# Performance work log

Measured on AMD Instinct MI355X. Metric: run time of the kernel, lower is better.

Reference implementation:

```python
import jax, jax.numpy as jnp
import numpy as np

B, T, C, H = 4, 4096, 1024, 16


def setup_inputs() -> dict:
    key = jax.random.key(0)
    k1, k2, k3 = jax.random.split(key, 3)
    x = jax.random.normal(k1, (B, T, C), dtype=jnp.float32)
    # nn.Linear(d_model, 3*d_model, bias=False): weight shape [3C, C]
    W_qkv = jax.random.normal(k2, (3 * C, C), dtype=jnp.float32) * 0.02
    # output Linear(d_model, d_model): weight [C, C], bias [C]
    W_out = jax.random.normal(k3, (C, C), dtype=jnp.float32) * 0.02
    b_out = jnp.zeros((C,), dtype=jnp.float32)
    return {"x": x, "W_qkv": W_qkv, "W_out": W_out, "b_out": b_out}


def reference(x, W_qkv, W_out, b_out):
    Bs, Ts, Cs = x.shape
    dh = Cs // H
    scale = dh ** (-0.5)
    # qkv projection: [B,T,3C]
    qkv = x @ W_qkv.T
    q, k, v = jnp.split(qkv, 3, axis=-1)

    def to_heads(t):  # [B,T,C] -> [B,H,T,dh]
        return t.reshape(Bs, Ts, H, dh).transpose(0, 2, 1, 3)

    q, k, v = to_heads(q), to_heads(k), to_heads(v)
    # rfft over the sequence dim -> [B,H,F,dh], F = T//2+1 (complex64)
    q_f = jnp.fft.rfft(q, axis=-2)
    k_f = jnp.fft.rfft(k, axis=-2)
    # spectral score: sum over head_dim of conj(q)*k, real part -> [B,H,F]
    attn = jnp.sum(jnp.conj(q_f) * k_f, axis=-1).real * scale
    attn = jax.nn.softmax(attn, axis=-1)  # softmax over frequency bins
    v_f = jnp.fft.rfft(v, axis=-2)
    out = jnp.fft.irfft(attn[..., None] * v_f, n=Ts, axis=-2)  # [B,H,T,dh]
    out = out.transpose(0, 2, 1, 3).reshape(Bs, Ts, Cs)
    # output projection (dropout is identity in eval)
    return out @ W_out.T + b_out
```

## Files before the change

kernel.cpp:

```cpp
#include <hip/hip_runtime.h>
#include <math.h>

#define Bsz   4
#define Tsz   4096
#define Csz   1024
#define Hn    16
#define DHn   64
#define NTOT  (Bsz * Tsz)
#define M3    (3 * Csz)
#define Fn    2049
#define BHn   (Bsz * Hn)
#define HALFN 8192

typedef __bf16 bf16x8 __attribute__((ext_vector_type(8)));
typedef __bf16 bf16x4 __attribute__((ext_vector_type(4)));
typedef float  f32x4  __attribute__((ext_vector_type(4)));

__device__ __forceinline__ void gload_lds16(const void* g, void* l) {
  __builtin_amdgcn_global_load_lds(
      (const __attribute__((address_space(1))) void*)g,
      (__attribute__((address_space(3))) void*)l, 16, 0, 0);
}

__global__ __launch_bounds__(256)
void cvt_hilo_kernel(const float4* __restrict__ in, bf16x4* __restrict__ hi,
                     bf16x4* __restrict__ lo, int n4) {
  int i = blockIdx.x * blockDim.x + threadIdx.x;
  if (i >= n4) return;
  float4 v = in[i];
  bf16x4 h, l;
  h[0] = (__bf16)v.x; h[1] = (__bf16)v.y; h[2] = (__bf16)v.z; h[3] = (__bf16)v.w;
  l[0] = (__bf16)(v.x - (float)h[0]);
  l[1] = (__bf16)(v.y - (float)h[1]);
  l[2] = (__bf16)(v.z - (float)h[2]);
  l[3] = (__bf16)(v.w - (float)h[3]);
  hi[i] = h;
  lo[i] = l;
}

__global__ __launch_bounds__(256)
void transpose_cvt_kernel(const float* __restrict__ src,
                          __bf16* __restrict__ hi, __bf16* __restrict__ lo) {
  __shared__ float tile[64][65];
  const int tid = threadIdx.x;
  const int n0 = blockIdx.x * 64;
  const int c0 = blockIdx.y * 64;
  const int col = tid & 63;
  const int row4 = tid >> 6;
#pragma unroll
  for (int i = 0; i < 16; ++i) {
    const int r = i * 4 + row4;
    tile[r][col] = src[(size_t)(c0 + r) * NTOT + n0 + col];
  }
  __syncthreads();
#pragma unroll
  for (int i = 0; i < 16; ++i) {
    const int n = i * 4 + row4;
    const float v = tile[col][n];
    const __bf16 h = (__bf16)v;
    const __bf16 l = (__bf16)(v - (float)h);
    hi[(size_t)(n0 + n) * Csz + c0 + col] = h;
    lo[(size_t)(n0 + n) * Csz + c0 + col] = l;
  }
}

template<int COLMAP>
__global__ __launch_bounds__(512, 2)
void gemm_8s(const __bf16* __restrict__ Ahi, const __bf16* __restrict__ Alo,
             const __bf16* __restrict__ Bhi, const __bf16* __restrict__ Blo,
             float* __restrict__ C, int ldC, int nbase,
             const float* __restrict__ bias) {
  __shared__ __align__(16) char lds[131072];

  const int tid  = threadIdx.x;
  const int wid  = tid >> 6;
  const int lane = tid & 63;
  const int wm = wid >> 2, wn = wid & 3;

  int bx = blockIdx.x, by = blockIdx.y;
  {
    const int gx = gridDim.x, gy = gridDim.y;
    const int nwg = gx * gy;
    if ((nwg & 7) == 0) {
      const int flat  = by * gx + bx;
      const int chunk = nwg >> 3;
      const int nf    = (flat & 7) * chunk + (flat >> 3);
      if (COLMAP) { bx = nf / gy; by = nf % gy; }
      else        { bx = nf % gx; by = nf / gx; }
    }
  }
  const int m0 = by * 256;
  const int n0 = bx * 256;

  const int r16 = lane & 15;
  const int kc  = lane >> 4;

  const int aq = (wid & 3) + ((wid & 4) ? 4 : 0);
  const int bq = ((wid & 3) << 1) + (wid >> 2);
  const __bf16* gAh = Ahi + (size_t)(m0 + (wid & 3) * 16 + ((wid & 4) ? 128 : 0) + r16) * Csz + kc * 8;
  const __bf16* gAl = Alo + (size_t)(m0 + (wid & 3) * 16 + ((wid & 4) ? 128 : 0) + r16) * Csz + kc * 8;
  const __bf16* gBh = Bhi + (size_t)(n0 + (wid & 3) * 64 + (wid >> 2) * 16 + r16) * Csz + kc * 8;
  const __bf16* gBl = Blo + (size_t)(n0 + (wid & 3) * 64 + (wid >> 2) * 16 + r16) * Csz + kc * 8;

  auto stA = [&](int h, int ts, char* slot) {
    const size_t o = (size_t)h * 64 * Csz + ts * 32;
    gload_lds16(gAh + o, slot + aq * 1024);
    gload_lds16(gAl + o, slot + 8192 + aq * 1024);
  };
  auto stB = [&](int h, int ts, char* slot) {
    const size_t o = (size_t)h * 32 * Csz + ts * 32;
    gload_lds16(gBh + o, slot + bq * 1024);
    gload_lds16(gBl + o, slot + 8192 + bq * 1024);
  };

  f32x4 acc[8][4];
#pragma unroll
  for (int i = 0; i < 8; ++i)
#pragma unroll
    for (int j = 0; j < 4; ++j) acc[i][j] = (f32x4)(0.f);

  stA(0, 0, lds);            stB(0, 0, lds + 16384);
  stB(1, 0, lds + 32768);    stA(1, 0, lds + 49152);
  stA(0, 1, lds + 65536);    stB(0, 1, lds + 81920);

#pragma unroll 1
  for (int t = 0; t < 32; ++t) {
    char* cur = lds + ((t & 1) << 16);
    char* nxt = lds + (((t & 1) ^ 1) << 16);
    bf16x8 ah[4], al[4], bh[4], bl[4];

    if (t < 31) asm volatile("s_waitcnt vmcnt(8)" ::: "memory");
    else        asm volatile("s_waitcnt vmcnt(4)" ::: "memory");
    __builtin_amdgcn_s_barrier();
#pragma unroll
    for (int f = 0; f < 4; ++f) {
      const int off = (wm * 4 + f) * 1024 + lane * 16;
      ah[f] = *(const bf16x8*)(cur + off);
      al[f] = *(const bf16x8*)(cur + 8192 + off);
    }
#pragma unroll
    for (int j = 0; j < 2; ++j) {
      const int off = ((wn << 1) + j) * 1024 + lane * 16;
      bh[j] = *(const bf16x8*)(cur + 16384 + off);
      bl[j] = *(const bf16x8*)(cur + 16384 + 8192 + off);
    }
    if (t < 31) stB(1, t + 1, nxt + 32768);
    asm volatile("s_waitcnt lgkmcnt(0)" ::: "memory");
    __builtin_amdgcn_sched_barrier(0);
    __builtin_amdgcn_s_setprio(1);
#pragma unroll
    for (int f = 0; f < 4; ++f)
#pragma unroll
      for (int j = 0; j < 2; ++j) {
        f32x4 a_ = acc[f][j];
        a_ = __builtin_amdgcn_mfma_f32_16x16x32_bf16(ah[f], bh[j], a_, 0, 0, 0);
        a_ = __builtin_amdgcn_mfma_f32_16x16x32_bf16(ah[f], bl[j], a_, 0, 0, 0);
        a_ = __builtin_amdgcn_mfma_f32_16x16x32_bf16(al[f], bh[j], a_, 0, 0, 0);
        acc[f][j] = a_;
      }
    __builtin_amdgcn_s_setprio(0);

    if (t < 31) asm volatile("s_waitcnt vmcnt(8)" ::: "memory");
    else        asm volatile("s_waitcnt vmcnt(2)" ::: "memory");
    __builtin_amdgcn_s_barrier();
#pragma unroll
    for (int j = 0; j < 2; ++j) {
      const int off = ((wn << 1) + j) * 1024 + lane * 16;
      bh[2 + j] = *(const bf16x8*)(cur + 32768 + off);
      bl[2 + j] = *(const bf16x8*)(cur + 32768 + 8192 + off);
    }
    if (t < 31) stA(1, t + 1, nxt + 49152);
    asm volatile("s_waitcnt lgkmcnt(0)" ::: "memory");
    __builtin_amdgcn_sched_barrier(0);
    __builtin_amdgcn_s_setprio(1);
#pragma unroll
    for (int f = 0; f < 4; ++f)
#pragma unroll
      for (int j = 0; j < 2; ++j) {
        f32x4 a_ = acc[f][2 + j];
        a_ = __builtin_amdgcn_mfma_f32_16x16x32_bf16(ah[f], bh[2 + j], a_, 0, 0, 0);
        a_ = __builtin_amdgcn_mfma_f32_16x16x32_bf16(ah[f], bl[2 + j], a_, 0, 0, 0);
        a_ = __builtin_amdgcn_mfma_f32_16x16x32_bf16(al[f], bh[2 + j], a_, 0, 0, 0);
        acc[f][2 + j] = a_;
      }
    __builtin_amdgcn_s_setprio(0);

    if (t < 31) asm volatile("s_waitcnt vmcnt(8)" ::: "memory");
    else        asm volatile("s_waitcnt vmcnt(0)" ::: "memory");
    __builtin_amdgcn_s_barrier();
#pragma unroll
    for (int f = 0; f < 4; ++f) {
      const int off = (wm * 4 + f) * 1024 + lane * 16;
      ah[f] = *(const bf16x8*)(cur + 49152 + off);
      al[f] = *(const bf16x8*)(cur + 49152 + 8192 + off);
    }
    if (t < 30) stA(0, t + 2, cur);
    asm volatile("s_waitcnt lgkmcnt(0)" ::: "memory");
    __builtin_amdgcn_sched_barrier(0);
    __builtin_amdgcn_s_setprio(1);
#pragma unroll
    for (int f = 0; f < 4; ++f)
#pragma unroll
      for (int j = 0; j < 2; ++j) {
        f32x4 a_ = acc[4 + f][j];
        a_ = __builtin_amdgcn_mfma_f32_16x16x32_bf16(ah[f], bh[j], a_, 0, 0, 0);
        a_ = __builtin_amdgcn_mfma_f32_16x16x32_bf16(ah[f], bl[j], a_, 0, 0, 0);
        a_ = __builtin_amdgcn_mfma_f32_16x16x32_bf16(al[f], bh[j], a_, 0, 0, 0);
        acc[4 + f][j] = a_;
      }
    __builtin_amdgcn_s_setprio(0);

    __builtin_amdgcn_s_barrier();
    if (t < 30) stB(0, t + 2, cur + 16384);
    __builtin_amdgcn_s_setprio(1);
#pragma unroll
    for (int f = 0; f < 4; ++f)
#pragma unroll
      for (int j = 0; j < 2; ++j) {
        f32x4 a_ = acc[4 + f][2 + j];
        a_ = __builtin_amdgcn_mfma_f32_16x16x32_bf16(ah[f], bh[2 + j], a_, 0, 0, 0);
        a_ = __builtin_amdgcn_mfma_f32_16x16x32_bf16(ah[f], bl[2 + j], a_, 0, 0, 0);
        a_ = __builtin_amdgcn_mfma_f32_16x16x32_bf16(al[f], bh[2 + j], a_, 0, 0, 0);
        acc[4 + f][2 + j] = a_;
      }
    __builtin_amdgcn_s_setprio(0);
  }

  const int cm = m0 + wm * 128 + (lane >> 4) * 4;
  const int cn = nbase + n0 + wn * 64 + (lane & 15);
  float bb[4];
#pragma unroll
  for (int g = 0; g < 4; ++g) bb[g] = bias ? bias[cn - nbase + g * 16] : 0.f;
#pragma unroll
  for (int fm = 0; fm < 8; ++fm)
#pragma unroll
    for (int r = 0; r < 4; ++r) {
      float* cp = C + (size_t)(cm + fm * 16 + r) * ldC + cn;
#pragma unroll
      for (int g = 0; g < 4; ++g) cp[g * 16] = acc[fm][g][r] + bb[g];
    }
}

template<int MF>
__global__ __launch_bounds__(512, 2)
void gemm_8p(const __bf16* __restrict__ Ahi, const __bf16* __restrict__ Alo,
             const __bf16* __restrict__ Bhi, const __bf16* __restrict__ Blo,
             float* __restrict__ C, int ldC, int nbase,
             const float* __restrict__ bias, int colmap) {
  constexpr int BM  = 32 * MF;
  constexpr int SA  = BM * 64;
  constexpr int SB  = 16384;
  constexpr int BUF = 2 * SA + 2 * SB;
  __shared__ __align__(16) char lds[2 * BUF];

  const int tid  = threadIdx.x;
  const int wid  = tid >> 6;
  const int lane = tid & 63;
  const int wm = wid >> 2, wn = wid & 3;

  int bx = blockIdx.x, by = blockIdx.y;
  {
    const int gx = gridDim.x, gy = gridDim.y;
    const int nwg = gx * gy;
    if ((nwg & 7) == 0) {
      const int flat  = by * gx + bx;
      const int chunk = nwg >> 3;
      const int nf    = (flat & 7) * chunk + (flat >> 3);
      if (colmap) { bx = nf / gy; by = nf % gy; }
      else        { bx = nf % gx; by = nf / gx; }
    }
  }
  const int m0 = by * BM;
  const int n0 = bx * 256;

  const int r16 = lane & 15;
  const int kc  = lane >> 4;

  const __bf16* gAh0 = Ahi + (size_t)(m0 + wid * 16 + r16) * Csz + kc * 8;
  const __bf16* gAl0 = Alo + (size_t)(m0 + wid * 16 + r16) * Csz + kc * 8;
  const __bf16* gBh0 = Bhi + (size_t)(n0 + wid * 16 + r16) * Csz + kc * 8;
  const __bf16* gBl0 = Blo + (size_t)(n0 + wid * 16 + r16) * Csz + kc * 8;
  const __bf16* gBh1 = gBh0 + (size_t)128 * Csz;
  const __bf16* gBl1 = gBl0 + (size_t)128 * Csz;
  const int dW = wid * 1024;

  f32x4 acc[MF][4];
#pragma unroll
  for (int i = 0; i < MF; ++i)
#pragma unroll
    for (int j = 0; j < 4; ++j) acc[i][j] = (f32x4)(0.f);

  auto stage = [&](char* base, int k0) {
    gload_lds16(gAh0 + k0, base + dW);
    gload_lds16(gAl0 + k0, base + SA + dW);
    gload_lds16(gBh0 + k0, base + 2 * SA + dW);
    gload_lds16(gBh1 + k0, base + 2 * SA + dW + 8192);
    gload_lds16(gBl0 + k0, base + 2 * SA + SB + dW);
    gload_lds16(gBl1 + k0, base + 2 * SA + SB + dW + 8192);
  };

  stage(lds, 0);

  for (int t = 0; t < 32; ++t) {
    char* buf = lds + (t & 1) * BUF;
    asm volatile("s_waitcnt vmcnt(0)" ::: "memory");
    __builtin_amdgcn_s_barrier();
    if (t < 31) stage(lds + ((t & 1) ^ 1) * BUF, (t + 1) * 32);

#pragma unroll
    for (int mh = 0; mh < 2; ++mh) {
      bf16x8 ah[MF / 2], al[MF / 2];
#pragma unroll
      for (int f = 0; f < MF / 2; ++f) {
        const int off = (wm * MF + mh * (MF / 2) + f) * 1024 + lane * 16;
        ah[f] = *(const bf16x8*)(buf + off);
        al[f] = *(const bf16x8*)(buf + SA + off);
      }
#pragma unroll
      for (int nh = 0; nh < 2; ++nh) {
        bf16x8 bh[2], bl[2];
#pragma unroll
        for (int g = 0; g < 2; ++g) {
          const int off = (wn * 4 + nh * 2 + g) * 1024 + lane * 16;
          bh[g] = *(const bf16x8*)(buf + 2 * SA + off);
          bl[g] = *(const bf16x8*)(buf + 2 * SA + SB + off);
        }
        asm volatile("s_waitcnt lgkmcnt(0)" ::: "memory");
        __builtin_amdgcn_sched_barrier(0);
        __builtin_amdgcn_s_setprio(1);
#pragma unroll
        for (int f = 0; f < MF / 2; ++f)
#pragma unroll
          for (int g = 0; g < 2; ++g) {
            f32x4 a_ = acc[mh * (MF / 2) + f][nh * 2 + g];
            a_ = __builtin_amdgcn_mfma_f32_16x16x32_bf16(ah[f], bh[g], a_, 0, 0, 0);
            a_ = __builtin_amdgcn_mfma_f32_16x16x32_bf16(ah[f], bl[g], a_, 0, 0, 0);
            a_ = __builtin_amdgcn_mfma_f32_16x16x32_bf16(al[f], bh[g], a_, 0, 0, 0);
            acc[mh * (MF / 2) + f][nh * 2 + g] = a_;
          }
        __builtin_amdgcn_s_setprio(0);
        __builtin_amdgcn_s_barrier();
      }
    }
  }

  const int cm = m0 + wm * (MF * 16) + (lane >> 4) * 4;
  const int cn = nbase + n0 + wn * 64 + (lane & 15);
  float bb[4];
#pragma unroll
  for (int g = 0; g < 4; ++g) bb[g] = bias ? bias[cn - nbase + g * 16] : 0.f;
#pragma unroll
  for (int fm = 0; fm < MF; ++fm)
#pragma unroll
    for (int r = 0; r < 4; ++r) {
      float* cp = C + (size_t)(cm + fm * 16 + r) * ldC + cn;
#pragma unroll
      for (int g = 0; g < 4; ++g) cp[g * 16] = acc[fm][g][r] + bb[g];
    }
}

__device__ __forceinline__ void build_twiddle(float2* tw, int tid) {
  const float k = 6.28318530717958647692f / 4096.0f;
#pragma unroll
  for (int i = 0; i < 4; ++i) {
    const int e = tid + (i << 8);
    float sn, cs;
    __sincosf(k * (float)e, &sn, &cs);
    tw[e] = make_float2(cs, sn);
  }
}

__device__ __forceinline__ float2 cmul(float2 a, float2 b) {
  return make_float2(a.x * b.x - a.y * b.y, a.x * b.y + a.y * b.x);
}

__device__ __forceinline__ void fft4096_r4(float2* X, float2* Y,
                                           const float2* __restrict__ tw,
                                           int tid, float sign) {
  float2* src = X;
  float2* dst = Y;
#pragma unroll 1
  for (int stage = 0; stage < 6; ++stage) {
    const int s = 1 << (2 * stage);
    __syncthreads();
#pragma unroll
    for (int it = 0; it < 4; ++it) {
      const int idx = tid + (it << 8);
      const int sp = idx & ~(s - 1);
      float2 a0 = src[idx];
      float2 a1 = src[idx + 1024];
      float2 a2 = src[idx + 2048];
      float2 a3 = src[idx + 3072];
      float2 b0 = make_float2(a0.x + a2.x, a0.y + a2.y);
      float2 b1 = make_float2(a0.x - a2.x, a0.y - a2.y);
      float2 b2 = make_float2(a1.x + a3.x, a1.y + a3.y);
      float2 b3 = make_float2(a1.x - a3.x, a1.y - a3.y);
      float2 y0 = make_float2(b0.x + b2.x, b0.y + b2.y);
      float2 y2 = make_float2(b0.x - b2.x, b0.y - b2.y);
      float2 y1 = make_float2(b1.x - sign * b3.y, b1.y + sign * b3.x);
      float2 y3 = make_float2(b1.x + sign * b3.y, b1.y - sign * b3.x);
      float2 w1 = tw[sp];
      w1.y *= sign;
      float2 w2 = make_float2(w1.x * w1.x - w1.y * w1.y, 2.f * w1.x * w1.y);
      float2 w3 = cmul(w1, w2);
      const int o = idx + 3 * sp;
      dst[o]         = y0;
      dst[o + s]     = cmul(w1, y1);
      dst[o + 2 * s] = cmul(w2, y2);
      dst[o + 3 * s] = cmul(w3, y3);
    }
    float2* t = src; src = dst; dst = t;
  }
  __syncthreads();
}

__global__ __launch_bounds__(256)
void qk_cross_kernel(const float* __restrict__ qkT, float* __restrict__ attn_raw,
                     int bhbase) {
  __shared__ float2 bufA[4096];
  __shared__ float2 bufB[4096];
  __shared__ float2 twid[1024];
  const int tid = threadIdx.x;
  const int blk = blockIdx.x;
  const int d = blk & 63;
  const int bh = bhbase + (blk >> 6);
  const int h = bh & 15;
  const int b = bh >> 4;

  build_twiddle(twid, tid);

  const float4* qrow = (const float4*)(qkT + (size_t)(h * DHn + d) * NTOT + b * Tsz);
  const float4* krow = (const float4*)(qkT + (size_t)(Csz + h * DHn + d) * NTOT + b * Tsz);
#pragma unroll
  for (int i = 0; i < 4; ++i) {
    const int t4 = tid + (i << 8);
    float4 qv = qrow[t4];
    float4 kv = krow[t4];
    bufA[t4 * 4 + 0] = make_float2(qv.x, kv.x);
    bufA[t4 * 4 + 1] = make_float2(qv.y, kv.y);
    bufA[t4 * 4 + 2] = make_float2(qv.z, kv.z);
    bufA[t4 * 4 + 3] = make_float2(qv.w, kv.w);
  }

  fft4096_r4(bufA, bufB, twid, tid, -1.0f);

  float* outp = attn_raw + (size_t)bh * Fn;
  for (int f = tid; f < Fn; f += 256) {
    float2 zf = bufA[f];
    float2 zn = bufA[(4096 - f) & 4095];
    float ar = zf.x + zn.x;
    float ai = zf.y - zn.y;
    float br = zf.x - zn.x;
    float bi = zf.y + zn.y;
    float val = 0.03125f * (ar * bi - ai * br);
    atomicAdd(&outp[f], val);
  }
}

__global__ __launch_bounds__(256)
void softmax_kernel(const float* __restrict__ raw, float* __restrict__ attn) {
  __shared__ float red[256];
  const int tid = threadIdx.x;
  const float* in = raw + (size_t)blockIdx.x * Fn;
  float* outp = attn + (size_t)blockIdx.x * Fn;

  float lmax = -3.4e38f;
  for (int f = tid; f < Fn; f += 256) lmax = fmaxf(lmax, in[f]);
  red[tid] = lmax;
  __syncthreads();
  for (int off = 128; off > 0; off >>= 1) {
    if (tid < off) red[tid] = fmaxf(red[tid], red[tid + off]);
    __syncthreads();
  }
  const float mx = red[0];
  __syncthreads();

  float lsum = 0.f;
  for (int f = tid; f < Fn; f += 256) lsum += __expf(in[f] - mx);
  red[tid] = lsum;
  __syncthreads();
  for (int off = 128; off > 0; off >>= 1) {
    if (tid < off) red[tid] += red[tid + off];
    __syncthreads();
  }
  const float inv = 1.0f / red[0];
  for (int f = tid; f < Fn; f += 256) outp[f] = __expf(in[f] - mx) * inv;
}

__global__ __launch_bounds__(256)
void v_filter_kernel(const float* __restrict__ vT, float* __restrict__ vbarT,
                     const float* __restrict__ attn) {
  __shared__ float2 bufA[4096];
  __shared__ float2 bufB[4096];
  __shared__ float2 twid[1024];
  const int tid = threadIdx.x;
  const int blk = blockIdx.x;
  const int jp = blk & 31;
  const int bh = blk >> 5;
  const int h = bh & 15;
  const int b = bh >> 4;
  const int d0 = jp * 2;

  build_twiddle(twid, tid);

  const float4* v0 = (const float4*)(vT + (size_t)(h * DHn + d0) * NTOT + b * Tsz);
  const float4* v1 = (const float4*)(vT + (size_t)(h * DHn + d0 + 1) * NTOT + b * Tsz);
#pragma unroll
  for (int i = 0; i < 4; ++i) {
    const int t4 = tid + (i << 8);
    float4 av = v0[t4];
    float4 bv = v1[t4];
    bufA[t4 * 4 + 0] = make_float2(av.x, bv.x);
    bufA[t4 * 4 + 1] = make_float2(av.y, bv.y);
    bufA[t4 * 4 + 2] = make_float2(av.z, bv.z);
    bufA[t4 * 4 + 3] = make_float2(av.w, bv.w);
  }

  fft4096_r4(bufA, bufB, twid, tid, -1.0f);

  const float* a = attn + (size_t)bh * Fn;
  for (int f = tid; f < 4096; f += 256) {
    int fm = (f <= 2048) ? f : (4096 - f);
    float s = a[fm];
    float2 z = bufA[f];
    bufA[f] = make_float2(z.x * s, z.y * s);
  }

  fft4096_r4(bufA, bufB, twid, tid, +1.0f);

  float* y0 = vbarT + (size_t)(h * DHn + d0) * NTOT + b * Tsz;
  float* y1 = y0 + NTOT;
  const float inv = 1.0f / 4096.0f;
  for (int t = tid; t < 4096; t += 256) {
    float2 z = bufA[t];
    y0[t] = z.x * inv;
    y1[t] = z.y * inv;
  }
}

__global__ void zero_kernel(float* __restrict__ p, int n) {
  int i = blockIdx.x * blockDim.x + threadIdx.x;
  if (i < n) p[i] = 0.f;
}

extern "C" void kernel_launch(void* const* d_in, const int* in_sizes, int n_in,
                              void* d_out, int out_size, void* d_ws, size_t ws_size,
                              hipStream_t stream) {
  const float* x    = (const float*)d_in[0];
  const float* Wqkv = (const float*)d_in[1];
  const float* Wout = (const float*)d_in[2];
  const float* bout = (const float*)d_in[3];
  float* out = (float*)d_out;

  char* ws = (char*)d_ws;
  float* qkT      = (float*)ws;
  float* vT       = (float*)ws;
  __bf16* VThi    = (__bf16*)ws;
  __bf16* VTlo    = (__bf16*)(ws + 33554432ull);
  float* vbarT    = (float*)(ws + 67108864ull);
  float* attn_raw = (float*)(ws + 134217728ull);
  float* attn     = (float*)(ws + 134742272ull);
  __bf16* Whi     = (__bf16*)(ws + 135266816ull);
  __bf16* Wlo     = (__bf16*)(ws + 141558272ull);
  __bf16* Xhi     = (__bf16*)(ws + 147849728ull);
  __bf16* Xlo     = (__bf16*)(ws + 164626944ull);
  __bf16* Wouthi  = (__bf16*)(ws + 181404160ull);
  __bf16* Woutlo  = (__bf16*)(ws + 183501312ull);

  const int nraw = BHn * Fn;
  zero_kernel<<<(nraw + 255) / 256, 256, 0, stream>>>(attn_raw, nraw);

  cvt_hilo_kernel<<<3072, 256, 0, stream>>>((const float4*)Wqkv,
                                            (bf16x4*)Whi, (bf16x4*)Wlo, 786432);
  cvt_hilo_kernel<<<1024, 256, 0, stream>>>((const float4*)Wout,
                                            (bf16x4*)Wouthi, (bf16x4*)Woutlo, 262144);

  for (int half = 0; half < 2; ++half) {
    cvt_hilo_kernel<<<8192, 256, 0, stream>>>(
        (const float4*)(x + (size_t)half * HALFN * Csz),
        (bf16x4*)Xhi, (bf16x4*)Xlo, 2097152);
    gemm_8s<1><<<dim3(32, 8), 512, 0, stream>>>(Whi, Wlo, Xhi, Xlo,
                                                qkT, NTOT, half * HALFN, nullptr);
    qk_cross_kernel<<<2048, 256, 0, stream>>>(qkT, attn_raw, half * 32);
    gemm_8p<4><<<dim3(32, 8), 512, 0, stream>>>(Whi + 2048 * Csz, Wlo + 2048 * Csz,
                                                Xhi, Xlo, vT, NTOT, half * HALFN,
                                                nullptr, 1);
  }

  softmax_kernel<<<BHn, 256, 0, stream>>>(attn_raw, attn);

  v_filter_kernel<<<2048, 256, 0, stream>>>(vT, vbarT, attn);

  transpose_cvt_kernel<<<dim3(NTOT / 64, Csz / 64), 256, 0, stream>>>(vbarT, VThi, VTlo);

  gemm_8s<0><<<dim3(4, 64), 512, 0, stream>>>(VThi, VTlo, Wouthi, Woutlo,
                                              out, Csz, 0, bout);
}
```

Before: 587.2 us.

## Prefetch GEMM fragments across phases and pad FFT shared buffers against bank conflicts

The 3-pass bf16 GEMM main loop is rescheduled: LDS fragment loads for the next phase, including the next k-step's A/B fragments, are now issued right after each MFMA block instead of before it. A deeper prefetch of stB(1) for step t+1 is added, and the vmcnt waits are recounted to match. Separately, the FFT shared buffers are padded with one float2 every 16 entries, so the strided radix-4 accesses no longer hit the same LDS banks. The changes add scheduling complexity and a little LDS per FFT block, and they risk wrong waitcnt accounting in the tail iterations.

After: 601.7 us. 1.02x slower.

```diff
diff --git a/kernel.cpp b/kernel.cpp
--- a/kernel.cpp
+++ b/kernel.cpp
@@ -15,6 +15,9 @@
 typedef __bf16 bf16x8 __attribute__((ext_vector_type(8)));
 typedef __bf16 bf16x4 __attribute__((ext_vector_type(4)));
 typedef float  f32x4  __attribute__((ext_vector_type(4)));
+
+#define VMCNT(n) asm volatile("s_waitcnt vmcnt(" #n ")" ::: "memory")
+#define LGKM0    asm volatile("s_waitcnt lgkmcnt(0)" ::: "memory")
 
 __device__ __forceinline__ void gload_lds16(const void* g, void* l) {
   __builtin_amdgcn_global_load_lds(
@@ -119,33 +122,33 @@
 #pragma unroll
     for (int j = 0; j < 4; ++j) acc[i][j] = (f32x4)(0.f);
 
+  bf16x8 ah[4], al[4], bh[4], bl[4];
+  const int offA = (wm * 4) * 1024 + lane * 16;
+  const int offB = (wn << 1) * 1024 + lane * 16;
+
   stA(0, 0, lds);            stB(0, 0, lds + 16384);
   stB(1, 0, lds + 32768);    stA(1, 0, lds + 49152);
-  stA(0, 1, lds + 65536);    stB(0, 1, lds + 81920);
+  stA(0, 1, lds + 65536);    stB(0, 1, lds + 65536 + 16384);
+  stB(1, 1, lds + 65536 + 32768);
+  VMCNT(8);
+  __builtin_amdgcn_s_barrier();
+#pragma unroll
+  for (int f = 0; f < 4; ++f) {
+    ah[f] = *(const bf16x8*)(lds + offA + f * 1024);
+    al[f] = *(const bf16x8*)(lds + 8192 + offA + f * 1024);
+  }
+#pragma unroll
+  for (int j = 0; j < 2; ++j) {
+    bh[j] = *(const bf16x8*)(lds + 16384 + offB + j * 1024);
+    bl[j] = *(const bf16x8*)(lds + 16384 + 8192 + offB + j * 1024);
+  }
 
 #pragma unroll 1
   for (int t = 0; t < 32; ++t) {
     char* cur = lds + ((t & 1) << 16);
     char* nxt = lds + (((t & 1) ^ 1) << 16);
-    bf16x8 ah[4], al[4], bh[4], bl[4];
-
-    if (t < 31) asm volatile("s_waitcnt vmcnt(8)" ::: "memory");
-    else        asm volatile("s_waitcnt vmcnt(4)" ::: "memory");
-    __builtin_amdgcn_s_barrier();
-#pragma unroll
-    for (int f = 0; f < 4; ++f) {
-      const int off = (wm * 4 + f) * 1024 + lane * 16;
-      ah[f] = *(const bf16x8*)(cur + off);
-      al[f] = *(const bf16x8*)(cur + 8192 + off);
-    }
-#pragma unroll
-    for (int j = 0; j < 2; ++j) {
-      const int off = ((wn << 1) + j) * 1024 + lane * 16;
-      bh[j] = *(const bf16x8*)(cur + 16384 + off);
-      bl[j] = *(const bf16x8*)(cur + 16384 + 8192 + off);
-    }
-    if (t < 31) stB(1, t + 1, nxt + 32768);
-    asm volatile("s_waitcnt lgkmcnt(0)" ::: "memory");
+
+    LGKM0;
     __builtin_amdgcn_sched_barrier(0);
     __builtin_amdgcn_s_setprio(1);
 #pragma unroll
@@ -159,18 +162,16 @@
         acc[f][j] = a_;
       }
     __builtin_amdgcn_s_setprio(0);
-
-    if (t < 31) asm volatile("s_waitcnt vmcnt(8)" ::: "memory");
-    else        asm volatile("s_waitcnt vmcnt(2)" ::: "memory");
+    if (t < 31) stA(1, t + 1, nxt + 49152);
+    if (t < 31) { VMCNT(8); } else { VMCNT(0); }
+#pragma unroll
+    for (int j = 0; j < 2; ++j) {
+      bh[2 + j] = *(const bf16x8*)(cur + 32768 + offB + j * 1024);
+      bl[2 + j] = *(const bf16x8*)(cur + 32768 + 8192 + offB + j * 1024);
+    }
     __builtin_amdgcn_s_barrier();
-#pragma unroll
-    for (int j = 0; j < 2; ++j) {
-      const int off = ((wn << 1) + j) * 1024 + lane * 16;
-      bh[2 + j] = *(const bf16x8*)(cur + 32768 + off);
-      bl[2 + j] = *(const bf16x8*)(cur + 32768 + 8192 + off);
-    }
-    if (t < 31) stA(1, t + 1, nxt + 49152);
-    asm volatile("s_waitcnt lgkmcnt(0)" ::: "memory");
+
+    LGKM0;
     __builtin_amdgcn_sched_barrier(0);
     __builtin_amdgcn_s_setprio(1);
 #pragma unroll
@@ -184,18 +185,16 @@
         acc[f][2 + j] = a_;
       }
     __builtin_amdgcn_s_setprio(0);
-
-    if (t < 31) asm volatile("s_waitcnt vmcnt(8)" ::: "memory");
-    else        asm volatile("s_waitcnt vmcnt(0)" ::: "memory");
+    if (t < 30) stA(0, t + 2, cur);
+    if (t < 30) { VMCNT(8); } else if (t == 30) { VMCNT(6); } else { VMCNT(0); }
+#pragma unroll
+    for (int f = 0; f < 4; ++f) {
+      ah[f] = *(const bf16x8*)(cur + 49152 + offA + f * 1024);
+      al[f] = *(const bf16x8*)(cur + 49152 + 8192 + offA + f * 1024);
+    }
     __builtin_amdgcn_s_barrier();
-#pragma unroll
-    for (int f = 0; f < 4; ++f) {
-      const int off = (wm * 4 + f) * 1024 + lane * 16;
-      ah[f] = *(const bf16x8*)(cur + 49152 + off);
-      al[f] = *(const bf16x8*)(cur + 49152 + 8192 + off);
-    }
-    if (t < 30) stA(0, t + 2, cur);
-    asm volatile("s_waitcnt lgkmcnt(0)" ::: "memory");
+
+    LGKM0;
     __builtin_amdgcn_sched_barrier(0);
     __builtin_amdgcn_s_setprio(1);
 #pragma unroll
@@ -209,9 +208,10 @@
         acc[4 + f][j] = a_;
       }
     __builtin_amdgcn_s_setprio(0);
-
+    if (t < 30) stB(0, t + 2, cur + 16384);
+    if (t < 30) { VMCNT(8); } else if (t == 30) { VMCNT(4); }
     __builtin_amdgcn_s_barrier();
-    if (t < 30) stB(0, t + 2, cur + 16384);
+
     __builtin_amdgcn_s_setprio(1);
 #pragma unroll
     for (int f = 0; f < 4; ++f)
@@ -224,6 +224,21 @@
         acc[4 + f][2 + j] = a_;
       }
     __builtin_amdgcn_s_setprio(0);
+    if (t < 30) stB(1, t + 2, cur + 32768);
+    if (t < 31) {
+      if (t < 30) { VMCNT(8); } else { VMCNT(2); }
+#pragma unroll
+      for (int f = 0; f < 4; ++f) {
+        ah[f] = *(const bf16x8*)(nxt + offA + f * 1024);
+        al[f] = *(const bf16x8*)(nxt + 8192 + offA + f * 1024);
+      }
+#pragma unroll
+      for (int j = 0; j < 2; ++j) {
+        bh[j] = *(const bf16x8*)(nxt + 16384 + offB + j * 1024);
+        bl[j] = *(const bf16x8*)(nxt + 16384 + 8192 + offB + j * 1024);
+      }
+      __builtin_amdgcn_s_barrier();
+    }
   }
 
   const int cm = m0 + wm * 128 + (lane >> 4) * 4;
@@ -303,7 +318,7 @@
 
   for (int t = 0; t < 32; ++t) {
     char* buf = lds + (t & 1) * BUF;
-    asm volatile("s_waitcnt vmcnt(0)" ::: "memory");
+    VMCNT(0);
     __builtin_amdgcn_s_barrier();
     if (t < 31) stage(lds + ((t & 1) ^ 1) * BUF, (t + 1) * 32);
 
@@ -325,7 +340,7 @@
           bh[g] = *(const bf16x8*)(buf + 2 * SA + off);
           bl[g] = *(const bf16x8*)(buf + 2 * SA + SB + off);
         }
-        asm volatile("s_waitcnt lgkmcnt(0)" ::: "memory");
+        LGKM0;
         __builtin_amdgcn_sched_barrier(0);
         __builtin_amdgcn_s_setprio(1);
 #pragma unroll
@@ -359,6 +374,9 @@
     }
 }
 
+#define PD(i) ((i) + ((i) >> 4))
+#define FFT_PAD_N 4352
+
 __device__ __forceinline__ void build_twiddle(float2* tw, int tid) {
   const float k = 6.28318530717958647692f / 4096.0f;
 #pragma unroll
@@ -387,10 +405,10 @@
     for (int it = 0; it < 4; ++it) {
       const int idx = tid + (it << 8);
       const int sp = idx & ~(s - 1);
-      float2 a0 = src[idx];
-      float2 a1 = src[idx + 1024];
-      float2 a2 = src[idx + 2048];
-      float2 a3 = src[idx + 3072];
+      float2 a0 = src[PD(idx)];
+      float2 a1 = src[PD(idx + 1024)];
+      float2 a2 = src[PD(idx + 2048)];
+      float2 a3 = src[PD(idx + 3072)];
       float2 b0 = make_float2(a0.x + a2.x, a0.y + a2.y);
       float2 b1 = make_float2(a0.x - a2.x, a0.y - a2.y);
       float2 b2 = make_float2(a1.x + a3.x, a1.y + a3.y);
@@ -404,10 +422,10 @@
       float2 w2 = make_float2(w1.x * w1.x - w1.y * w1.y, 2.f * w1.x * w1.y);
       float2 w3 = cmul(w1, w2);
       const int o = idx + 3 * sp;
-      dst[o]         = y0;
-      dst[o + s]     = cmul(w1, y1);
-      dst[o + 2 * s] = cmul(w2, y2);
-      dst[o + 3 * s] = cmul(w3, y3);
+      dst[PD(o)]         = y0;
+      dst[PD(o + s)]     = cmul(w1, y1);
+      dst[PD(o + 2 * s)] = cmul(w2, y2);
+      dst[PD(o + 3 * s)] = cmul(w3, y3);
     }
     float2* t = src; src = dst; dst = t;
   }
@@ -417,8 +435,8 @@
 __global__ __launch_bounds__(256)
 void qk_cross_kernel(const float* __restrict__ qkT, float* __restrict__ attn_raw,
                      int bhbase) {
-  __shared__ float2 bufA[4096];
-  __shared__ float2 bufB[4096];
+  __shared__ float2 bufA[FFT_PAD_N];
+  __shared__ float2 bufB[FFT_PAD_N];
   __shared__ float2 twid[1024];
   const int tid = threadIdx.x;
   const int blk = blockIdx.x;
@@ -436,18 +454,18 @@
     const int t4 = tid + (i << 8);
     float4 qv = qrow[t4];
     float4 kv = krow[t4];
-    bufA[t4 * 4 + 0] = make_float2(qv.x, kv.x);
-    bufA[t4 * 4 + 1] = make_float2(qv.y, kv.y);
-    bufA[t4 * 4 + 2] = make_float2(qv.z, kv.z);
-    bufA[t4 * 4 + 3] = make_float2(qv.w, kv.w);
+    bufA[PD(t4 * 4 + 0)] = make_float2(qv.x, kv.x);
+    bufA[PD(t4 * 4 + 1)] = make_float2(qv.y, kv.y);
+    bufA[PD(t4 * 4 + 2)] = make_float2(qv.z, kv.z);
+    bufA[PD(t4 * 4 + 3)] = make_float2(qv.w, kv.w);
   }
 
   fft4096_r4(bufA, bufB, twid, tid, -1.0f);
 
   float* outp = attn_raw + (size_t)bh * Fn;
   for (int f = tid; f < Fn; f += 256) {
-    float2 zf = bufA[f];
-    float2 zn = bufA[(4096 - f) & 4095];
+    float2 zf = bufA[PD(f)];
+    float2 zn = bufA[PD((4096 - f) & 4095)];
     float ar = zf.x + zn.x;
     float ai = zf.y - zn.y;
     float br = zf.x - zn.x;
@@ -490,8 +508,8 @@
 __global__ __launch_bounds__(256)
 void v_filter_kernel(const float* __restrict__ vT, float* __restrict__ vbarT,
                      const float* __restrict__ attn) {
-  __shared__ float2 bufA[4096];
-  __shared__ float2 bufB[4096];
+  __shared__ float2 bufA[FFT_PAD_N];
+  __shared__ float2 bufB[FFT_PAD_N];
   __shared__ float2 twid[1024];
   const int tid = threadIdx.x;
   const int blk = blockIdx.x;
@@ -510,10 +528,10 @@
     const int t4 = tid + (i << 8);
     float4 av = v0[t4];
     float4 bv = v1[t4];
-    bufA[t4 * 4 + 0] = make_float2(av.x, bv.x);
-    bufA[t4 * 4 + 1] = make_float2(av.y, bv.y);
-    bufA[t4 * 4 + 2] = make_float2(av.z, bv.z);
-    bufA[t4 * 4 + 3] = make_float2(av.w, bv.w);
+    bufA[PD(t4 * 4 + 0)] = make_float2(av.x, bv.x);
+    bufA[PD(t4 * 4 + 1)] = make_float2(av.y, bv.y);
+    bufA[PD(t4 * 4 + 2)] = make_float2(av.z, bv.z);
+    bufA[PD(t4 * 4 + 3)] = make_float2(av.w, bv.w);
   }
 
   fft4096_r4(bufA, bufB, twid, tid, -1.0f);
@@ -522,8 +540,8 @@
   for (int f = tid; f < 4096; f += 256) {
     int fm = (f <= 2048) ? f : (4096 - f);
     float s = a[fm];
-    float2 z = bufA[f];
-    bufA[f] = make_float2(z.x * s, z.y * s);
+    float2 z = bufA[PD(f)];
+    bufA[PD(f)] = make_float2(z.x * s, z.y * s);
   }
 
   fft4096_r4(bufA, bufB, twid, tid, +1.0f);
@@ -532,7 +550,7 @@
   float* y1 = y0 + NTOT;
   const float inv = 1.0f / 4096.0f;
   for (int t = tid; t < 4096; t += 256) {
-    float2 z = bufA[t];
+    float2 z = bufA[PD(t)];
     y0[t] = z.x * inv;
     y1[t] = z.y * inv;
   }
```
